# Optimization experiments

Hardware: AMD Instinct MI355X
Metric: run time of the kernel (lower is better)

Reference implementation:

```python
import jax, jax.numpy as jnp
import numpy as np

NUM_HEADS = 16
THETA = 10000.0


def apply_rope(x, positions, theta=THETA):
    # x: [B, H, S, d_k], positions: [B, S] (broadcast over heads)
    d_k = x.shape[-1]
    inv_freq = theta ** (-jnp.arange(0, d_k // 2, dtype=jnp.float32) * 2.0 / d_k)  # [d_k/2]
    ang = positions[:, None, :, None].astype(jnp.float32) * inv_freq  # [B,1,S,d_k/2]
    cos, sin = jnp.cos(ang), jnp.sin(ang)
    x1 = x[..., 0::2]
    x2 = x[..., 1::2]
    r1 = x1 * cos - x2 * sin
    r2 = x1 * sin + x2 * cos
    # interleave back: [..., d_k/2, 2] -> [..., d_k]
    return jnp.stack([r1, r2], axis=-1).reshape(x.shape)


def setup_inputs() -> dict:
    key = jax.random.key(0)
    ks = jax.random.split(key, 5)
    B, S, D = 1, 4096, 1024
    scale = 1.0 / np.sqrt(D)
    x = jax.random.normal(ks[0], (B, S, D), dtype=jnp.float32)
    Wq = jax.random.normal(ks[1], (D, D), dtype=jnp.float32) * scale
    Wk = jax.random.normal(ks[2], (D, D), dtype=jnp.float32) * scale
    Wv = jax.random.normal(ks[3], (D, D), dtype=jnp.float32) * scale
    Wo = jax.random.normal(ks[4], (D, D), dtype=jnp.float32) * scale
    token_positions = jnp.broadcast_to(jnp.arange(S, dtype=jnp.int32), (B, S))
    return {"x": x, "token_positions": token_positions, "Wq": Wq, "Wk": Wk, "Wv": Wv, "Wo": Wo}


def reference(x, token_positions, Wq, Wk, Wv, Wo):
    B, S, D = x.shape
    H = NUM_HEADS
    d_k = D // H
    # fused QKV projection (Linear: y = x @ W^T, no bias)
    q = jnp.einsum('bsd,ed->bse', x, Wq)
    k = jnp.einsum('bsd,ed->bse', x, Wk)
    v = jnp.einsum('bsd,ed->bse', x, Wv)
    # [B,S,H*dk] -> [B,H,S,dk]
    Q = q.reshape(B, S, H, d_k).transpose(0, 2, 1, 3)
    K = k.reshape(B, S, H, d_k).transpose(0, 2, 1, 3)
    V = v.reshape(B, S, H, d_k).transpose(0, 2, 1, 3)
    Q = apply_rope(Q, token_positions)
    K = apply_rope(K, token_positions)
    scores = jnp.einsum('bhqd,bhkd->bhqk', Q, K) / jnp.sqrt(jnp.float32(d_k))
    causal = jnp.tril(jnp.ones((S, S), dtype=bool))
    scores = jnp.where(causal, scores, -jnp.inf)
    P = jax.nn.softmax(scores, axis=-1)
    out = jnp.einsum('bhqk,bhkd->bhqd', P, V)  # [B,H,S,dk]
    out = out.transpose(0, 2, 1, 3).reshape(B, S, D)
    return jnp.einsum('bsd,ed->bse', out, Wo)
```

## Files before the change

kernel.cpp:

```cpp
#include <hip/hip_runtime.h>
#include <hip/hip_bf16.h>
#include <stdint.h>
#include <math.h>

#define S_LEN   4096
#define D_MODEL 1024
#define NHEAD   16
#define DK      64

typedef __attribute__((ext_vector_type(8))) __bf16 bf16x8;
typedef __attribute__((ext_vector_type(4))) float  f32x4;
using bf16 = __hip_bfloat16;

__device__ __forceinline__ void load_lds16(const bf16* g, bf16* l) {
    __builtin_amdgcn_global_load_lds(
        (const __attribute__((address_space(1))) void*)g,
        (__attribute__((address_space(3))) void*)l, 16, 0, 0);
}

__global__ void cvt_all(const float* __restrict__ x,
                        const float* __restrict__ w0, const float* __restrict__ w1,
                        const float* __restrict__ w2, const float* __restrict__ w3,
                        bf16* __restrict__ xb,
                        bf16* __restrict__ b0, bf16* __restrict__ b1,
                        bf16* __restrict__ b2, bf16* __restrict__ b3)
{
    size_t i4 = ((size_t)blockIdx.x * 256 + threadIdx.x) * 4;
    const float* s; bf16* d; size_t off;
    const size_t NX = (size_t)S_LEN * D_MODEL;
    const size_t NW = (size_t)D_MODEL * D_MODEL;
    if (i4 < NX) { s = x; d = xb; off = i4; }
    else {
        size_t j = i4 - NX;
        int sel = (int)(j >> 20);
        off = j & (NW - 1);
        s = sel == 0 ? w0 : sel == 1 ? w1 : sel == 2 ? w2 : w3;
        d = sel == 0 ? b0 : sel == 1 ? b1 : sel == 2 ? b2 : b3;
    }
    float4 v = *(const float4*)&s[off];
    bf16 t[4] __attribute__((aligned(8)));
    t[0] = __float2bfloat16(v.x); t[1] = __float2bfloat16(v.y);
    t[2] = __float2bfloat16(v.z); t[3] = __float2bfloat16(v.w);
    *(uint64_t*)&d[off] = *(const uint64_t*)t;
}

__global__ __launch_bounds__(256) void qkv_gemm(
    const bf16* __restrict__ Xb,
    const bf16* __restrict__ Wq, const bf16* __restrict__ Wk, const bf16* __restrict__ Wv,
    const int* __restrict__ pos,
    bf16* __restrict__ Qb, bf16* __restrict__ Kb, bf16* __restrict__ VtG)
{
    const int K = D_MODEL, N = D_MODEL;
    int z = blockIdx.z;
    const bf16* B = (z == 0) ? Wq : (z == 1) ? Wk : Wv;

    __shared__ __align__(16) bf16 As[2][128 * 32];
    __shared__ __align__(16) bf16 Bs[2][128 * 32];
    __shared__ __align__(16) bf16 Ts[4][64 * 24];

    int row0 = blockIdx.y * 128;
    int col0 = blockIdx.x * 128;
    int tid  = threadIdx.x;
    int wv   = tid >> 6, lane = tid & 63;
    int m16  = lane & 15, quad = lane >> 4;
    int wr   = (wv >> 1) * 64, wc = (wv & 1) * 64;
    int l4   = lane >> 2, l3 = (lane & 3) * 8;

    const bf16* ga_base = Xb + (size_t)(row0 + wv * 16 + l4) * K + l3;
    const bf16* gb_base = B  + (size_t)(col0 + wv * 16 + l4) * K + l3;

    auto stage = [&](int k0, int buf) {
        load_lds16(ga_base + k0,            &As[buf][wv * 512]);
        load_lds16(ga_base + k0 + 64 * K,   &As[buf][2048 + wv * 512]);
        load_lds16(gb_base + k0,            &Bs[buf][wv * 512]);
        load_lds16(gb_base + k0 + 64 * K,   &Bs[buf][2048 + wv * 512]);
    };

    f32x4 acc[4][4];
    #pragma unroll
    for (int i = 0; i < 4; i++)
        #pragma unroll
        for (int j = 0; j < 4; j++) acc[i][j] = (f32x4){0.f, 0.f, 0.f, 0.f};

    stage(0, 0);
    for (int k0 = 0; k0 < K; k0 += 32) {
        __syncthreads();
        int buf = (k0 >> 5) & 1;
        if (k0 + 32 < K) stage(k0 + 32, buf ^ 1);
        bf16x8 a[4], b[4];
        #pragma unroll
        for (int mi = 0; mi < 4; mi++) a[mi] = *(const bf16x8*)&As[buf][(wr + mi * 16 + m16) * 32 + quad * 8];
        #pragma unroll
        for (int ni = 0; ni < 4; ni++) b[ni] = *(const bf16x8*)&Bs[buf][(wc + ni * 16 + m16) * 32 + quad * 8];
        #pragma unroll
        for (int mi = 0; mi < 4; mi++)
            #pragma unroll
            for (int ni = 0; ni < 4; ni++)
                acc[mi][ni] = __builtin_amdgcn_mfma_f32_16x16x32_bf16(a[mi], b[ni], acc[mi][ni], 0, 0, 0);
    }

    if (z < 2) {
        bf16* O = (z == 0) ? Qb : Kb;
        const float qscale = (z == 0) ? 0.18033688011112042f : 1.0f;
        float invf[4];
        #pragma unroll
        for (int ni = 0; ni < 4; ni++) {
            float fi = (float)((ni * 16 + m16) >> 1);
            invf[ni] = exp2f(fi * (-0.41524101186092028f));
        }
        bool odd = (m16 & 1) != 0;
        #pragma unroll
        for (int mi = 0; mi < 4; mi++) {
            #pragma unroll
            for (int r = 0; r < 4; r++) {
                int gr = row0 + wr + mi * 16 + quad * 4 + r;
                float p = (float)pos[gr];
                #pragma unroll
                for (int ni = 0; ni < 4; ni++) {
                    float own   = acc[mi][ni][r];
                    float other = __shfl_xor(own, 1);
                    float sn, cs;
                    __sincosf(p * invf[ni], &sn, &cs);
                    float x1 = odd ? other : own;
                    float x2 = odd ? own   : other;
                    float res = odd ? (x1 * sn + x2 * cs) : (x1 * cs - x2 * sn);
                    int gc = col0 + wc + ni * 16 + m16;
                    O[(size_t)gr * N + gc] = __float2bfloat16(res * qscale);
                }
            }
        }
    } else {
        #pragma unroll
        for (int mi = 0; mi < 4; mi++) {
            #pragma unroll
            for (int nt = 0; nt < 4; nt++) {
                bf16 t4[4] __attribute__((aligned(8)));
                #pragma unroll
                for (int r = 0; r < 4; r++) t4[r] = __float2bfloat16(acc[mi][nt][r]);
                *(uint64_t*)&Ts[wv][(nt * 16 + m16) * 24 + quad * 4] = *(const uint64_t*)t4;
            }
            #pragma unroll
            for (int rep = 0; rep < 2; rep++) {
                int c  = (lane >> 1) + rep * 32;
                int r8 = lane & 1;
                bf16x8 val = *(const bf16x8*)&Ts[wv][c * 24 + r8 * 8];
                int gc = col0 + wc + c;
                int gr = row0 + wr + mi * 16 + r8 * 8;
                *(bf16x8*)&VtG[(size_t)gc * S_LEN + gr] = val;
            }
        }
    }
}

__global__ __launch_bounds__(256) void out_gemm(
    const bf16* __restrict__ A_, const bf16* __restrict__ B,
    float* __restrict__ C)
{
    const int K = D_MODEL, N = D_MODEL;
    __shared__ __align__(16) bf16 As[2][128 * 32];
    __shared__ __align__(16) bf16 Bs[2][64 * 32];

    int row0 = blockIdx.y * 128;
    int col0 = blockIdx.x * 64;
    int tid  = threadIdx.x;
    int wv   = tid >> 6, lane = tid & 63;
    int m16  = lane & 15, quad = lane >> 4;
    int wr   = (wv >> 1) * 64, wc = (wv & 1) * 32;
    int l4   = lane >> 2, l3 = (lane & 3) * 8;

    const bf16* ga_base = A_ + (size_t)(row0 + wv * 16 + l4) * K + l3;
    const bf16* gb_base = B  + (size_t)(col0 + wv * 16 + l4) * K + l3;

    auto stage = [&](int k0, int buf) {
        load_lds16(ga_base + k0,            &As[buf][wv * 512]);
        load_lds16(ga_base + k0 + 64 * K,   &As[buf][2048 + wv * 512]);
        load_lds16(gb_base + k0,            &Bs[buf][wv * 512]);
    };

    f32x4 acc[4][2];
    #pragma unroll
    for (int i = 0; i < 4; i++)
        #pragma unroll
        for (int j = 0; j < 2; j++) acc[i][j] = (f32x4){0.f, 0.f, 0.f, 0.f};

    stage(0, 0);
    for (int k0 = 0; k0 < K; k0 += 32) {
        __syncthreads();
        int buf = (k0 >> 5) & 1;
        if (k0 + 32 < K) stage(k0 + 32, buf ^ 1);
        bf16x8 a[4], b[2];
        #pragma unroll
        for (int mi = 0; mi < 4; mi++) a[mi] = *(const bf16x8*)&As[buf][(wr + mi * 16 + m16) * 32 + quad * 8];
        #pragma unroll
        for (int ni = 0; ni < 2; ni++) b[ni] = *(const bf16x8*)&Bs[buf][(wc + ni * 16 + m16) * 32 + quad * 8];
        #pragma unroll
        for (int mi = 0; mi < 4; mi++)
            #pragma unroll
            for (int ni = 0; ni < 2; ni++)
                acc[mi][ni] = __builtin_amdgcn_mfma_f32_16x16x32_bf16(a[mi], b[ni], acc[mi][ni], 0, 0, 0);
    }

    #pragma unroll
    for (int mi = 0; mi < 4; mi++)
        #pragma unroll
        for (int ni = 0; ni < 2; ni++)
            #pragma unroll
            for (int r = 0; r < 4; r++) {
                int gr = row0 + wr + mi * 16 + quad * 4 + r;
                int gc = col0 + wc + ni * 16 + m16;
                C[(size_t)gr * N + gc] = acc[mi][ni][r];
            }
}

__global__ __launch_bounds__(256, 4) void attn_kernel(
    const bf16* __restrict__ Qb, const bf16* __restrict__ Kb, const bf16* __restrict__ VtG,
    bf16* __restrict__ Attn)
{
    int bx  = blockIdx.x;
    int h   = bx & 15;
    int qt  = 63 - (bx >> 4);
    int tid = threadIdx.x;
    int wv  = tid >> 6, lane = tid & 63;
    int m16 = lane & 15, quad = lane >> 4;
    int csw   = (lane & 3) ^ ((lane >> 3) & 3);
    int colsw = ((quad ^ ((m16 >> 1) & 3)) << 3);
    int psw   = (m16 & 7) ^ ((m16 >> 3) & 1);
    int hc  = h * DK;
    int q0  = qt * 64;

    __shared__ __align__(16) bf16 KT[2][2][64 * 32];
    __shared__ __align__(16) bf16 VT[2][2][64 * 32];
    __shared__ __align__(16) bf16 Ps[64 * 64];

    const bf16* kgl = Kb  + (size_t)(wv * 16 + (lane >> 2)) * D_MODEL + hc + csw * 8;
    const bf16* vgl = VtG + (size_t)(hc + wv * 16 + (lane >> 2)) * S_LEN + csw * 8;

    auto stage = [&](int kb, int buf) {
        size_t ko = (size_t)kb * 64;
        load_lds16(kgl + ko * D_MODEL,       &KT[buf][0][wv * 512]);
        load_lds16(kgl + ko * D_MODEL + 32,  &KT[buf][1][wv * 512]);
        load_lds16(vgl + ko,                 &VT[buf][0][wv * 512]);
        load_lds16(vgl + ko + 32,            &VT[buf][1][wv * 512]);
    };

    const bf16* qp = Qb + (size_t)(q0 + wv * 16 + m16) * D_MODEL + hc;
    bf16x8 aq0 = *(const bf16x8*)&qp[quad * 8];
    bf16x8 aq1 = *(const bf16x8*)&qp[32 + quad * 8];

    bf16x8 bone;
    #pragma unroll
    for (int j = 0; j < 8; j++) bone[j] = (__bf16)1.0f;

    f32x4 o[4];
    f32x4 o_sum = (f32x4){0.f, 0.f, 0.f, 0.f};
    #pragma unroll
    for (int dt = 0; dt < 4; dt++) o[dt] = (f32x4){0.f, 0.f, 0.f, 0.f};

    const float SHIFT = 8.0f;
    const int myq = q0 + wv * 16 + m16;
    const int psrow = (wv * 16 + m16) * 64;

    stage(0, 0);
    for (int kb = 0; kb <= qt; ++kb) {
        __syncthreads();
        int buf = kb & 1;
        if (kb < qt) stage(kb + 1, buf ^ 1);
        int kbase = kb * 64;
        bool diag = (kb == qt);

        #pragma unroll
        for (int nt = 0; nt < 4; nt++) {
            bf16x8 k0 = *(const bf16x8*)&KT[buf][0][(nt * 16 + m16) * 32 + colsw];
            bf16x8 k1 = *(const bf16x8*)&KT[buf][1][(nt * 16 + m16) * 32 + colsw];
            f32x4 zv = (f32x4){0.f, 0.f, 0.f, 0.f};
            zv = __builtin_amdgcn_mfma_f32_16x16x32_bf16(k0, aq0, zv, 0, 0, 0);
            zv = __builtin_amdgcn_mfma_f32_16x16x32_bf16(k1, aq1, zv, 0, 0, 0);

            bf16 t4[4] __attribute__((aligned(8)));
            #pragma unroll
            for (int r = 0; r < 4; r++) {
                float pv = __builtin_amdgcn_exp2f(zv[r] - SHIFT);
                if (diag) {
                    int key = kbase + nt * 16 + quad * 4 + r;
                    if (key > myq) pv = 0.f;
                }
                t4[r] = __float2bfloat16(pv);
            }
            int cw = (nt * 2 + (quad >> 1)) ^ psw;
            *(uint64_t*)&Ps[psrow + cw * 8 + (quad & 1) * 4] = *(const uint64_t*)t4;
        }

        int c0 = quad ^ psw;
        bf16x8 ap0 = *(const bf16x8*)&Ps[psrow + c0 * 8];
        bf16x8 ap1 = *(const bf16x8*)&Ps[psrow + (c0 ^ 4) * 8];

        #pragma unroll
        for (int dt = 0; dt < 4; dt++) {
            bf16x8 v0 = *(const bf16x8*)&VT[buf][0][(dt * 16 + m16) * 32 + colsw];
            bf16x8 v1 = *(const bf16x8*)&VT[buf][1][(dt * 16 + m16) * 32 + colsw];
            o[dt] = __builtin_amdgcn_mfma_f32_16x16x32_bf16(ap0, v0, o[dt], 0, 0, 0);
            o[dt] = __builtin_amdgcn_mfma_f32_16x16x32_bf16(ap1, v1, o[dt], 0, 0, 0);
        }
        o_sum = __builtin_amdgcn_mfma_f32_16x16x32_bf16(ap0, bone, o_sum, 0, 0, 0);
        o_sum = __builtin_amdgcn_mfma_f32_16x16x32_bf16(ap1, bone, o_sum, 0, 0, 0);
    }

    #pragma unroll
    for (int r = 0; r < 4; r++) {
        float inv = 1.0f / o_sum[r];
        int rowg = q0 + wv * 16 + quad * 4 + r;
        #pragma unroll
        for (int dt = 0; dt < 4; dt++)
            Attn[(size_t)rowg * D_MODEL + hc + dt * 16 + m16] =
                __float2bfloat16(o[dt][r] * inv);
    }
}

extern "C" void kernel_launch(void* const* d_in, const int* in_sizes, int n_in,
                              void* d_out, int out_size, void* d_ws, size_t ws_size,
                              hipStream_t stream)
{
    const float* x  = (const float*)d_in[0];
    const int*   pos= (const int*)d_in[1];
    const float* Wq = (const float*)d_in[2];
    const float* Wk = (const float*)d_in[3];
    const float* Wv = (const float*)d_in[4];
    const float* Wo = (const float*)d_in[5];
    float* out = (float*)d_out;

    char* ws = (char*)d_ws;
    bf16*  xb   = (bf16*) (ws);
    bf16*  wqb  = (bf16*) (ws + ( 8ull << 20));
    bf16*  wkb  = (bf16*) (ws + (10ull << 20));
    bf16*  wvb  = (bf16*) (ws + (12ull << 20));
    bf16*  wob  = (bf16*) (ws + (14ull << 20));
    bf16*  Qb   = (bf16*) (ws + (16ull << 20));
    bf16*  Kb   = (bf16*) (ws + (24ull << 20));
    bf16*  VtG  = (bf16*) (ws + (32ull << 20));
    bf16*  Attn = (bf16*) (ws + (40ull << 20));

    cvt_all<<<8192, 256, 0, stream>>>(x, Wq, Wk, Wv, Wo, xb, wqb, wkb, wvb, wob);

    qkv_gemm<<<dim3(8, 32, 3), 256, 0, stream>>>(xb, wqb, wkb, wvb, pos, Qb, Kb, VtG);

    attn_kernel<<<dim3(1024), 256, 0, stream>>>(Qb, Kb, VtG, Attn);

    out_gemm<<<dim3(16, 32), 256, 0, stream>>>(Attn, wob, out);
}
```

Before: 210.9 us.

## Rewrite attention with 32x32 MFMA, register-resident P, and split-K across wave pairs

The attention kernel changes from 16x16 MFMA tiles with K/V staged through LDS to 32x32x16 MFMA tiles. Each wave loads K and V fragments directly from global memory, and P stays in registers via packed bf16 conversion instead of a round trip through LDS. Each 32-query block is split across two waves that process alternating key tiles, and their partial outputs and row sums are merged through LDS at the end. This removes the per-iteration barriers, the LDS staging, and the extra ones-MFMA used for the row sum. In exchange, K/V reads go uncached through global/L2 with no reuse across waves, and loads are no longer prefetched asynchronously.

```diff
diff --git a/kernel.cpp b/kernel.cpp
--- a/kernel.cpp
+++ b/kernel.cpp
@@ -8,8 +8,10 @@
 #define NHEAD   16
 #define DK      64
 
-typedef __attribute__((ext_vector_type(8))) __bf16 bf16x8;
-typedef __attribute__((ext_vector_type(4))) float  f32x4;
+typedef __attribute__((ext_vector_type(8)))  __bf16 bf16x8;
+typedef __attribute__((ext_vector_type(4)))  float  f32x4;
+typedef __attribute__((ext_vector_type(16))) float  f32x16;
+typedef __attribute__((ext_vector_type(4)))  unsigned int u32x4;
 using bf16 = __hip_bfloat16;
 
 __device__ __forceinline__ void load_lds16(const bf16* g, bf16* l) {
@@ -221,98 +223,106 @@
     int qt  = 63 - (bx >> 4);
     int tid = threadIdx.x;
     int wv  = tid >> 6, lane = tid & 63;
-    int m16 = lane & 15, quad = lane >> 4;
-    int csw   = (lane & 3) ^ ((lane >> 3) & 3);
-    int colsw = ((quad ^ ((m16 >> 1) & 3)) << 3);
-    int psw   = (m16 & 7) ^ ((m16 >> 3) & 1);
+    int wq  = wv >> 1, wp = wv & 1;
+    int l31 = lane & 31, hi = lane >> 5;
     int hc  = h * DK;
-    int q0  = qt * 64;
-
-    __shared__ __align__(16) bf16 KT[2][2][64 * 32];
-    __shared__ __align__(16) bf16 VT[2][2][64 * 32];
-    __shared__ __align__(16) bf16 Ps[64 * 64];
-
-    const bf16* kgl = Kb  + (size_t)(wv * 16 + (lane >> 2)) * D_MODEL + hc + csw * 8;
-    const bf16* vgl = VtG + (size_t)(hc + wv * 16 + (lane >> 2)) * S_LEN + csw * 8;
-
-    auto stage = [&](int kb, int buf) {
-        size_t ko = (size_t)kb * 64;
-        load_lds16(kgl + ko * D_MODEL,       &KT[buf][0][wv * 512]);
-        load_lds16(kgl + ko * D_MODEL + 32,  &KT[buf][1][wv * 512]);
-        load_lds16(vgl + ko,                 &VT[buf][0][wv * 512]);
-        load_lds16(vgl + ko + 32,            &VT[buf][1][wv * 512]);
+    int qs  = qt * 64 + wq * 32;
+    int m   = qs >> 5;
+    int myq = qs + l31;
+
+    __shared__ float Obuf[2][2][16][64];
+    __shared__ float Lbuf[2][2][32];
+
+    int krow = (l31 & 19) | (((l31 >> 3) & 1) << 2) | (((l31 >> 2) & 1) << 3);
+
+    const bf16* kb_base = Kb  + (size_t)krow * D_MODEL + hc + hi * 8;
+    const bf16* q_base  = Qb  + (size_t)(qs + l31) * D_MODEL + hc + hi * 8;
+    const bf16* v_base  = VtG + (size_t)(hc + l31) * S_LEN + hi * 8;
+
+    bf16x8 aQ[4];
+    #pragma unroll
+    for (int d = 0; d < 4; d++) aQ[d] = *(const bf16x8*)&q_base[d * 16];
+
+    f32x16 o0, o1;
+    #pragma unroll
+    for (int i = 0; i < 16; i++) { o0[i] = 0.f; o1[i] = 0.f; }
+    float l_part = 0.f;
+
+    auto tile = [&](int kt, bool diag) {
+        int kb = kt * 32;
+        const bf16* kp = kb_base + (size_t)kb * D_MODEL;
+        bf16x8 aK0 = *(const bf16x8*)&kp[0];
+        bf16x8 aK1 = *(const bf16x8*)&kp[16];
+        bf16x8 aK2 = *(const bf16x8*)&kp[32];
+        bf16x8 aK3 = *(const bf16x8*)&kp[48];
+        const bf16* vp = v_base + kb;
+        bf16x8 bV00 = *(const bf16x8*)&vp[0];
+        bf16x8 bV10 = *(const bf16x8*)&vp[16];
+        bf16x8 bV01 = *(const bf16x8*)&vp[(size_t)32 * S_LEN];
+        bf16x8 bV11 = *(const bf16x8*)&vp[(size_t)32 * S_LEN + 16];
+
+        f32x16 s;
+        #pragma unroll
+        for (int i = 0; i < 16; i++) s[i] = 0.f;
+        s = __builtin_amdgcn_mfma_f32_32x32x16_bf16(aK0, aQ[0], s, 0, 0, 0);
+        s = __builtin_amdgcn_mfma_f32_32x32x16_bf16(aK1, aQ[1], s, 0, 0, 0);
+        s = __builtin_amdgcn_mfma_f32_32x32x16_bf16(aK2, aQ[2], s, 0, 0, 0);
+        s = __builtin_amdgcn_mfma_f32_32x32x16_bf16(aK3, aQ[3], s, 0, 0, 0);
+
+        float p[16];
+        #pragma unroll
+        for (int r = 0; r < 16; r++) {
+            float pv = __builtin_amdgcn_exp2f(s[r] - 8.0f);
+            if (diag) {
+                int key = kb + (r & 3) + ((r >> 2) & 1) * 4 + hi * 8 + (r >> 3) * 16;
+                if (key > myq) pv = 0.f;
+            }
+            l_part += pv;
+            p[r] = pv;
+        }
+
+        unsigned int w[8];
+        #pragma unroll
+        for (int i = 0; i < 8; i++)
+            asm("v_cvt_pk_bf16_f32 %0, %1, %2" : "=v"(w[i]) : "v"(p[2 * i]), "v"(p[2 * i + 1]));
+        u32x4 wa = {w[0], w[1], w[2], w[3]};
+        u32x4 wb = {w[4], w[5], w[6], w[7]};
+        bf16x8 aP0 = __builtin_bit_cast(bf16x8, wa);
+        bf16x8 aP1 = __builtin_bit_cast(bf16x8, wb);
+
+        o0 = __builtin_amdgcn_mfma_f32_32x32x16_bf16(aP0, bV00, o0, 0, 0, 0);
+        o0 = __builtin_amdgcn_mfma_f32_32x32x16_bf16(aP1, bV10, o0, 0, 0, 0);
+        o1 = __builtin_amdgcn_mfma_f32_32x32x16_bf16(aP0, bV01, o1, 0, 0, 0);
+        o1 = __builtin_amdgcn_mfma_f32_32x32x16_bf16(aP1, bV11, o1, 0, 0, 0);
     };
 
-    const bf16* qp = Qb + (size_t)(q0 + wv * 16 + m16) * D_MODEL + hc;
-    bf16x8 aq0 = *(const bf16x8*)&qp[quad * 8];
-    bf16x8 aq1 = *(const bf16x8*)&qp[32 + quad * 8];
-
-    bf16x8 bone;
-    #pragma unroll
-    for (int j = 0; j < 8; j++) bone[j] = (__bf16)1.0f;
-
-    f32x4 o[4];
-    f32x4 o_sum = (f32x4){0.f, 0.f, 0.f, 0.f};
-    #pragma unroll
-    for (int dt = 0; dt < 4; dt++) o[dt] = (f32x4){0.f, 0.f, 0.f, 0.f};
-
-    const float SHIFT = 8.0f;
-    const int myq = q0 + wv * 16 + m16;
-    const int psrow = (wv * 16 + m16) * 64;
-
-    stage(0, 0);
-    for (int kb = 0; kb <= qt; ++kb) {
-        __syncthreads();
-        int buf = kb & 1;
-        if (kb < qt) stage(kb + 1, buf ^ 1);
-        int kbase = kb * 64;
-        bool diag = (kb == qt);
-
-        #pragma unroll
-        for (int nt = 0; nt < 4; nt++) {
-            bf16x8 k0 = *(const bf16x8*)&KT[buf][0][(nt * 16 + m16) * 32 + colsw];
-            bf16x8 k1 = *(const bf16x8*)&KT[buf][1][(nt * 16 + m16) * 32 + colsw];
-            f32x4 zv = (f32x4){0.f, 0.f, 0.f, 0.f};
-            zv = __builtin_amdgcn_mfma_f32_16x16x32_bf16(k0, aq0, zv, 0, 0, 0);
-            zv = __builtin_amdgcn_mfma_f32_16x16x32_bf16(k1, aq1, zv, 0, 0, 0);
-
-            bf16 t4[4] __attribute__((aligned(8)));
-            #pragma unroll
-            for (int r = 0; r < 4; r++) {
-                float pv = __builtin_amdgcn_exp2f(zv[r] - SHIFT);
-                if (diag) {
-                    int key = kbase + nt * 16 + quad * 4 + r;
-                    if (key > myq) pv = 0.f;
-                }
-                t4[r] = __float2bfloat16(pv);
-            }
-            int cw = (nt * 2 + (quad >> 1)) ^ psw;
-            *(uint64_t*)&Ps[psrow + cw * 8 + (quad & 1) * 4] = *(const uint64_t*)t4;
-        }
-
-        int c0 = quad ^ psw;
-        bf16x8 ap0 = *(const bf16x8*)&Ps[psrow + c0 * 8];
-        bf16x8 ap1 = *(const bf16x8*)&Ps[psrow + (c0 ^ 4) * 8];
-
-        #pragma unroll
-        for (int dt = 0; dt < 4; dt++) {
-            bf16x8 v0 = *(const bf16x8*)&VT[buf][0][(dt * 16 + m16) * 32 + colsw];
-            bf16x8 v1 = *(const bf16x8*)&VT[buf][1][(dt * 16 + m16) * 32 + colsw];
-            o[dt] = __builtin_amdgcn_mfma_f32_16x16x32_bf16(ap0, v0, o[dt], 0, 0, 0);
-            o[dt] = __builtin_amdgcn_mfma_f32_16x16x32_bf16(ap1, v1, o[dt], 0, 0, 0);
-        }
-        o_sum = __builtin_amdgcn_mfma_f32_16x16x32_bf16(ap0, bone, o_sum, 0, 0, 0);
-        o_sum = __builtin_amdgcn_mfma_f32_16x16x32_bf16(ap1, bone, o_sum, 0, 0, 0);
-    }
-
-    #pragma unroll
-    for (int r = 0; r < 4; r++) {
-        float inv = 1.0f / o_sum[r];
-        int rowg = q0 + wv * 16 + quad * 4 + r;
-        #pragma unroll
-        for (int dt = 0; dt < 4; dt++)
-            Attn[(size_t)rowg * D_MODEL + hc + dt * 16 + m16] =
-                __float2bfloat16(o[dt][r] * inv);
+    int nfull = (m - wp + 1) >> 1;
+    for (int i = 0; i < nfull; i++) tile(wp + 2 * i, false);
+    if ((m & 1) == wp) tile(m, true);
+
+    float lt = l_part + __shfl_xor(l_part, 32);
+
+    if (wp == 1) {
+        #pragma unroll
+        for (int r = 0; r < 16; r++) {
+            Obuf[wq][0][r][lane] = o0[r];
+            Obuf[wq][1][r][lane] = o1[r];
+        }
+    }
+    if (lane < 32) Lbuf[wq][wp][lane] = lt;
+    __syncthreads();
+    if (wp == 0) {
+        #pragma unroll
+        for (int r = 0; r < 16; r++) {
+            int qr = (r & 3) + (r >> 2) * 8 + hi * 4;
+            float lsum = Lbuf[wq][0][qr] + Lbuf[wq][1][qr];
+            float inv  = 1.0f / lsum;
+            float v0 = (o0[r] + Obuf[wq][0][r][lane]) * inv;
+            float v1 = (o1[r] + Obuf[wq][1][r][lane]) * inv;
+            bf16* dst = Attn + (size_t)(qs + qr) * D_MODEL + hc + l31;
+            dst[0]  = __float2bfloat16(v0);
+            dst[32] = __float2bfloat16(v1);
+        }
     }
 }
 
```

New measurement: 289.5 us. +37.3%, slower.
